# Performance work log

Measured on AMD Instinct MI355X. Metric: run time of the kernel, lower is better.

Reference implementation:

```python
import jax, jax.numpy as jnp
import numpy as np

N_NODES = 50000
N_EDGES = 800000
F_IN, F_MID, F_OUT = 256, 128, 40


def gcn_conv(x, W, b, src, dst, n_nodes):
    # GCNConv (PyG defaults): add self-loops, symmetric normalization,
    # linear transform, scatter-sum to targets, then bias.
    h = x @ W  # [N, F_out]
    loop = jnp.arange(n_nodes, dtype=src.dtype)
    s = jnp.concatenate([src, loop])  # sources incl. self-loops
    d = jnp.concatenate([dst, loop])  # targets incl. self-loops
    deg = jax.ops.segment_sum(jnp.ones_like(d, dtype=h.dtype), d, num_segments=n_nodes)
    dinv = jnp.where(deg > 0, jax.lax.rsqrt(deg), 0.0)
    norm = dinv[s] * dinv[d]  # [E+N]
    msgs = h[s] * norm[:, None]  # [E+N, F_out]
    out = jax.ops.segment_sum(msgs, d, num_segments=n_nodes)
    return out + b


def setup_inputs() -> dict:
    key = jax.random.key(0)
    ks = jax.random.split(key, 8)
    x = jax.random.normal(ks[0], (N_NODES, F_IN), dtype=jnp.float32)
    edge_index = jax.random.randint(ks[1], (2, N_EDGES), 0, N_NODES, dtype=jnp.int64)

    def glorot(k, fin, fout):
        lim = float(np.sqrt(6.0 / (fin + fout)))
        return jax.random.uniform(k, (fin, fout), jnp.float32, -lim, lim)

    return {
        "x": x,
        "edge_index": edge_index,
        "W_in": glorot(ks[2], F_IN, F_MID),
        "b_in": jnp.zeros((F_MID,), jnp.float32),
        "W_mid": glorot(ks[3], F_MID, F_MID),
        "b_mid": jnp.zeros((F_MID,), jnp.float32),
        "W_out": glorot(ks[4], F_MID, F_OUT),
        "b_out": jnp.zeros((F_OUT,), jnp.float32),
    }


def reference(x, edge_index, W_in, b_in, W_mid, b_mid, W_out, b_out):
    src, dst = edge_index[0], edge_index[1]
    n = x.shape[0]
    # conv_in -> relu (dropout is identity in eval mode)
    h = jax.nn.relu(gcn_conv(x, W_in, b_in, src, dst, n))
    # middle GCN layer -> relu
    h = jax.nn.relu(gcn_conv(h, W_mid, b_mid, src, dst, n))
    # conv_out -> log_softmax over classes
    h = gcn_conv(h, W_out, b_out, src, dst, n)
    return jax.nn.log_softmax(h, axis=-1)
```

## Files before the change

### kernel.cpp

```cpp
#include <hip/hip_runtime.h>
#include <hip/hip_bf16.h>
#include <math.h>


#define F_IN  256
#define F_MID 128
#define F_OUT 40
#define PSH   9
#define BCAP2 10240

typedef __attribute__((ext_vector_type(8))) short bf16x8;
typedef __attribute__((ext_vector_type(4))) float f32x4;

union FragU {
    bf16x8 v;
    __hip_bfloat162 h2[4];
    uint4 u;
    unsigned short s[8];
};

__device__ __forceinline__ unsigned int f2bf(float f) {
    unsigned int u = __float_as_uint(f);
    return (u + 0x7fffu + ((u >> 16) & 1u)) >> 16;
}
__device__ __forceinline__ float bf_lo(unsigned int u) { return __uint_as_float(u << 16); }
__device__ __forceinline__ float bf_hi(unsigned int u) { return __uint_as_float(u & 0xffff0000u); }

__global__ __launch_bounds__(256) void k_bucket_prep(const int* __restrict__ src,
                                                     const int* __restrict__ dst,
                                                     unsigned int* __restrict__ bkt,
                                                     int* __restrict__ bcur,
                                                     int E, int nbB,
                                                     const float* __restrict__ W1,
                                                     const float* __restrict__ W2,
                                                     const float* __restrict__ W3,
                                                     unsigned short* __restrict__ Wp1,
                                                     unsigned short* __restrict__ Wp2,
                                                     unsigned short* __restrict__ Wp3) {
    if (blockIdx.x >= (unsigned)nbB) {
        int t = (blockIdx.x - nbB) * 256 + threadIdx.x;
        const float* W; unsigned short* Wp; int M, Mp, kc, nn;
        if (t < 4096)      { W = W1; Wp = Wp1; M = 128; Mp = 128; kc = t >> 7; nn = t & 127; }
        else if (t < 6144) { t -= 4096; W = W2; Wp = Wp2; M = 128; Mp = 128; kc = t >> 7; nn = t & 127; }
        else if (t < 6912) { t -= 6144; W = W3; Wp = Wp3; M = 40;  Mp = 48;  kc = t / 48; nn = t % 48; }
        else return;
        FragU o;
#pragma unroll
        for (int j = 0; j < 8; ++j) {
            int k = kc * 8 + j;
            o.s[j] = (nn < M) ? (unsigned short)f2bf(W[k * M + nn]) : 0;
        }
        *(uint4*)&Wp[((size_t)kc * Mp + nn) * 8] = o.u;
        return;
    }
    __shared__ int hist[128], base[128], cur[128];
    const int ntiles = (E + 2047) >> 11;
    for (int tile = blockIdx.x; tile < ntiles; tile += nbB) {
        const int e0 = tile << 11;
        if (threadIdx.x < 128) { hist[threadIdx.x] = 0; cur[threadIdx.x] = 0; }
        __syncthreads();
        int myp[8];
        unsigned int mye[8];
#pragma unroll
        for (int j = 0; j < 8; ++j) {
            int e = e0 + j * 256 + threadIdx.x;
            myp[j] = -1;
            if (e < E) {
                int s = src[e], d = dst[e];
                int p = d >> PSH;
                myp[j] = p;
                mye[j] = ((unsigned int)d << 16) | (unsigned int)s;
                atomicAdd(&hist[p], 1);
            }
        }
        __syncthreads();
        if (threadIdx.x < 128)
            base[threadIdx.x] = atomicAdd(&bcur[threadIdx.x], hist[threadIdx.x]);
        __syncthreads();
#pragma unroll
        for (int j = 0; j < 8; ++j) {
            if (myp[j] >= 0) {
                int p = myp[j];
                int pos = base[p] + atomicAdd(&cur[p], 1);
                if (pos < BCAP2) bkt[(size_t)p * BCAP2 + pos] = mye[j];
            }
        }
        __syncthreads();
    }
}

__global__ __launch_bounds__(256) void k_gemm1_sort(const unsigned int* __restrict__ bkt,
                                                    const int* __restrict__ bcur,
                                                    int* __restrict__ rofs,
                                                    float* __restrict__ dinv,
                                                    unsigned short* __restrict__ csr,
                                                    int nbG, int npart,
                                                    const float* __restrict__ x,
                                                    const unsigned short* __restrict__ Wp1,
                                                    unsigned short* __restrict__ hn, int n) {
    if (blockIdx.x >= (unsigned)nbG) {
        __shared__ int hist[512];
        __shared__ int stmp[256];
        const int p = blockIdx.x - nbG;
        const int t = threadIdx.x;
        const int d0 = p << PSH;
        const int nd = min(512, n - d0);

        int bv = (t < p) ? bcur[t] : 0;
        bv = bv > BCAP2 ? BCAP2 : bv;
        stmp[t] = bv;
        hist[t] = 0; hist[t + 256] = 0;
        __syncthreads();
#pragma unroll
        for (int off = 128; off; off >>= 1) {
            if (t < off) stmp[t] += stmp[t + off];
            __syncthreads();
        }
        const int base = stmp[0];
        int np = bcur[p]; np = np > BCAP2 ? BCAP2 : np;
        const unsigned int* b = bkt + (size_t)p * BCAP2;

        for (int i = t; i < np; i += 256)
            atomicAdd(&hist[(int)(b[i] >> 16) - d0], 1);
        __syncthreads();

        const int h0 = hist[2 * t], h1 = hist[2 * t + 1];
        __syncthreads();
        stmp[t] = h0 + h1;
        __syncthreads();
#pragma unroll
        for (int off = 1; off < 256; off <<= 1) {
            int xx = (t >= off) ? stmp[t - off] : 0;
            __syncthreads();
            stmp[t] += xx;
            __syncthreads();
        }
        const int excl = stmp[t] - (h0 + h1);

        hist[2 * t] = excl;
        hist[2 * t + 1] = excl + h0;
        if (2 * t < nd) {
            rofs[d0 + 2 * t] = base + excl;
            dinv[d0 + 2 * t] = rsqrtf((float)(h0 + 1));
        }
        if (2 * t + 1 < nd) {
            rofs[d0 + 2 * t + 1] = base + excl + h0;
            dinv[d0 + 2 * t + 1] = rsqrtf((float)(h1 + 1));
        }
        if (p == npart - 1 && t == 0) rofs[n] = base + np;
        __syncthreads();

        for (int i = t; i < np; i += 256) {
            unsigned int en = b[i];
            int ld = (int)(en >> 16) - d0;
            int pos = atomicAdd(&hist[ld], 1);
            csr[base + pos] = (unsigned short)(en & 0xffffu);
        }
        return;
    }
    const int t = threadIdx.x;
    const int w = t >> 6, lane = t & 63, sub = lane & 15, q = lane >> 4;
    const int row0 = blockIdx.x * 64 + w * 16;
    const int row = row0 + sub;
    const bool rv = row < n;
    const float* ap = x + (size_t)row * 256;

    float4 xv[16];
    if (rv) {
#pragma unroll
        for (int j = 0; j < 16; ++j)
            xv[j] = *(const float4*)(ap + (j >> 1) * 32 + q * 8 + (j & 1) * 4);
    } else {
#pragma unroll
        for (int j = 0; j < 16; ++j) xv[j] = make_float4(0.f, 0.f, 0.f, 0.f);
    }

    f32x4 acc[8];
#pragma unroll
    for (int cg = 0; cg < 8; ++cg) acc[cg] = (f32x4)0.f;

#pragma unroll
    for (int kk = 0; kk < 8; ++kk) {
        FragU af;
        float4 f0 = xv[2 * kk];
        float4 f1 = xv[2 * kk + 1];
        af.h2[0] = __float22bfloat162_rn(make_float2(f0.x, f0.y));
        af.h2[1] = __float22bfloat162_rn(make_float2(f0.z, f0.w));
        af.h2[2] = __float22bfloat162_rn(make_float2(f1.x, f1.y));
        af.h2[3] = __float22bfloat162_rn(make_float2(f1.z, f1.w));
        const unsigned short* wrow = Wp1 + (size_t)((kk * 4 + q) * 128 + sub) * 8;
#pragma unroll
        for (int cg = 0; cg < 8; ++cg) {
            bf16x8 b = *(const bf16x8*)(wrow + cg * 16 * 8);
            acc[cg] = __builtin_amdgcn_mfma_f32_16x16x32_bf16(af.v, b, acc[cg], 0, 0, 0);
        }
    }

    const int rbase = row0 + q * 4;
#pragma unroll
    for (int cg = 0; cg < 8; ++cg)
#pragma unroll
        for (int r = 0; r < 4; ++r) {
            int rr = rbase + r;
            if (rr < n)
                hn[(size_t)rr * 128 + cg * 16 + sub] = (unsigned short)f2bf(acc[cg][r]);
        }
}

template <int K>
__global__ __launch_bounds__(256) void gemm_mfma_bf16A(const unsigned short* __restrict__ A,
                                                       const unsigned short* __restrict__ Wp,
                                                       unsigned short* __restrict__ hn, int n) {
    const int t = threadIdx.x;
    const int w = t >> 6, lane = t & 63, sub = lane & 15, q = lane >> 4;
    const int row0 = blockIdx.x * 64 + w * 16;
    const int row = row0 + sub;
    const bool rv = row < n;
    const unsigned short* ap = A + (size_t)row * K;

    uint4 xv[K / 32];
    if (rv) {
#pragma unroll
        for (int j = 0; j < K / 32; ++j)
            xv[j] = *(const uint4*)(ap + j * 32 + q * 8);
    } else {
#pragma unroll
        for (int j = 0; j < K / 32; ++j) xv[j] = make_uint4(0, 0, 0, 0);
    }

    f32x4 acc[8];
#pragma unroll
    for (int cg = 0; cg < 8; ++cg) acc[cg] = (f32x4)0.f;

#pragma unroll
    for (int kk = 0; kk < K / 32; ++kk) {
        FragU af; af.u = xv[kk];
        const unsigned short* wrow = Wp + (size_t)((kk * 4 + q) * 128 + sub) * 8;
#pragma unroll
        for (int cg = 0; cg < 8; ++cg) {
            bf16x8 b = *(const bf16x8*)(wrow + cg * 16 * 8);
            acc[cg] = __builtin_amdgcn_mfma_f32_16x16x32_bf16(af.v, b, acc[cg], 0, 0, 0);
        }
    }

    const int rbase = row0 + q * 4;
#pragma unroll
    for (int cg = 0; cg < 8; ++cg)
#pragma unroll
        for (int r = 0; r < 4; ++r) {
            int rr = rbase + r;
            if (rr < n)
                hn[(size_t)rr * 128 + cg * 16 + sub] = (unsigned short)f2bf(acc[cg][r]);
        }
}

__global__ __launch_bounds__(256) void gemm_mfma_m40(const unsigned short* __restrict__ A,
                                                     const unsigned short* __restrict__ Wp,
                                                     unsigned short* __restrict__ hn, int n) {
    const int K = 128;
    const int t = threadIdx.x;
    const int w = t >> 6, lane = t & 63, sub = lane & 15, q = lane >> 4;
    const int row0 = blockIdx.x * 64 + w * 16;
    const int row = row0 + sub;
    const bool rv = row < n;
    const unsigned short* ap = A + (size_t)row * K;

    uint4 xv[4];
    if (rv) {
#pragma unroll
        for (int j = 0; j < 4; ++j)
            xv[j] = *(const uint4*)(ap + j * 32 + q * 8);
    } else {
#pragma unroll
        for (int j = 0; j < 4; ++j) xv[j] = make_uint4(0, 0, 0, 0);
    }

    f32x4 acc[3];
#pragma unroll
    for (int cg = 0; cg < 3; ++cg) acc[cg] = (f32x4)0.f;

#pragma unroll
    for (int kk = 0; kk < 4; ++kk) {
        FragU af; af.u = xv[kk];
        const unsigned short* wrow = Wp + (size_t)((kk * 4 + q) * 48 + sub) * 8;
#pragma unroll
        for (int cg = 0; cg < 3; ++cg) {
            bf16x8 b = *(const bf16x8*)(wrow + cg * 16 * 8);
            acc[cg] = __builtin_amdgcn_mfma_f32_16x16x32_bf16(af.v, b, acc[cg], 0, 0, 0);
        }
    }

    const int rbase = row0 + q * 4;
#pragma unroll
    for (int cg = 0; cg < 3; ++cg) {
        int col = cg * 16 + sub;
        if (col < 40) {
#pragma unroll
            for (int r = 0; r < 4; ++r) {
                int rr = rbase + r;
                if (rr < n)
                    hn[(size_t)rr * 40 + col] = (unsigned short)f2bf(acc[cg][r]);
            }
        }
    }
}

__device__ __forceinline__ void acc_row(float* acc, uint4 u, float dv) {
    acc[0] += dv * bf_lo(u.x); acc[1] += dv * bf_hi(u.x);
    acc[2] += dv * bf_lo(u.y); acc[3] += dv * bf_hi(u.y);
    acc[4] += dv * bf_lo(u.z); acc[5] += dv * bf_hi(u.z);
    acc[6] += dv * bf_lo(u.w); acc[7] += dv * bf_hi(u.w);
}

__global__ __launch_bounds__(256) void agg128_bf16(const unsigned short* __restrict__ hn,
                                                   const int* __restrict__ rofs,
                                                   const unsigned short* __restrict__ csr,
                                                   const float* __restrict__ dinv,
                                                   const float* __restrict__ bias,
                                                   unsigned short* __restrict__ obf, int n) {
    int wid = (blockIdx.x * 256 + threadIdx.x) >> 6;
    if (wid >= n) return;
    const int v = wid;
    const int lane = threadIdx.x & 63;
    const int q = lane >> 4;
    const int sub = lane & 15;
    float acc[8];
#pragma unroll
    for (int k = 0; k < 8; ++k) acc[k] = 0.f;
    const int e0 = rofs[v];
    const int total = rofs[v + 1] - e0 + 1;
    int i = q;
    for (; i + 12 < total; i += 16) {
        int s0 = (i == 0) ? v : (int)csr[e0 + i - 1];
        int s1 = (int)csr[e0 + i + 3];
        int s2 = (int)csr[e0 + i + 7];
        int s3 = (int)csr[e0 + i + 11];
        float d0 = dinv[s0], d1 = dinv[s1], d2 = dinv[s2], d3 = dinv[s3];
        uint4 u0 = *(const uint4*)(hn + (size_t)s0 * 128 + sub * 8);
        uint4 u1 = *(const uint4*)(hn + (size_t)s1 * 128 + sub * 8);
        uint4 u2 = *(const uint4*)(hn + (size_t)s2 * 128 + sub * 8);
        uint4 u3 = *(const uint4*)(hn + (size_t)s3 * 128 + sub * 8);
        acc_row(acc, u0, d0); acc_row(acc, u1, d1);
        acc_row(acc, u2, d2); acc_row(acc, u3, d3);
    }
    for (; i < total; i += 4) {
        int s = (i == 0) ? v : (int)csr[e0 + i - 1];
        float d = dinv[s];
        uint4 u = *(const uint4*)(hn + (size_t)s * 128 + sub * 8);
        acc_row(acc, u, d);
    }
#pragma unroll
    for (int k = 0; k < 8; ++k) {
        acc[k] += __shfl_xor(acc[k], 16);
        acc[k] += __shfl_xor(acc[k], 32);
    }
    if (q == 0) {
        float dv = dinv[v];
        float4 b0 = *(const float4*)(bias + sub * 8);
        float4 b1 = *(const float4*)(bias + sub * 8 + 4);
        float o[8];
        o[0] = fmaxf(dv * acc[0] + b0.x, 0.f);
        o[1] = fmaxf(dv * acc[1] + b0.y, 0.f);
        o[2] = fmaxf(dv * acc[2] + b0.z, 0.f);
        o[3] = fmaxf(dv * acc[3] + b0.w, 0.f);
        o[4] = fmaxf(dv * acc[4] + b1.x, 0.f);
        o[5] = fmaxf(dv * acc[5] + b1.y, 0.f);
        o[6] = fmaxf(dv * acc[6] + b1.z, 0.f);
        o[7] = fmaxf(dv * acc[7] + b1.w, 0.f);
        uint4 pk;
        pk.x = f2bf(o[0]) | (f2bf(o[1]) << 16);
        pk.y = f2bf(o[2]) | (f2bf(o[3]) << 16);
        pk.z = f2bf(o[4]) | (f2bf(o[5]) << 16);
        pk.w = f2bf(o[6]) | (f2bf(o[7]) << 16);
        *(uint4*)(obf + (size_t)v * 128 + sub * 8) = pk;
    }
}

__global__ __launch_bounds__(256) void agg40_lsm_bf16(const unsigned short* __restrict__ hn,
                                                      const int* __restrict__ rofs,
                                                      const unsigned short* __restrict__ csr,
                                                      const float* __restrict__ dinv,
                                                      const float* __restrict__ bias,
                                                      float* __restrict__ out, int n) {
    int wid = (blockIdx.x * 256 + threadIdx.x) >> 6;
    if (wid >= n) return;
    const int v = wid;
    const int lane = threadIdx.x & 63;
    const int h = lane >> 5;
    const int sl = lane & 31;
    const bool act = sl < 20;
    float a0 = 0.f, a1 = 0.f;
    const int e0 = rofs[v];
    const int total = rofs[v + 1] - e0 + 1;
    int i = h;
    for (; i + 2 < total; i += 4) {
        int s0 = (i == 0) ? v : (int)csr[e0 + i - 1];
        int s1 = (int)csr[e0 + i + 1];
        if (act) {
            float d0 = dinv[s0], d1 = dinv[s1];
            unsigned int u0 = *(const unsigned int*)(hn + (size_t)s0 * 40 + sl * 2);
            unsigned int u1 = *(const unsigned int*)(hn + (size_t)s1 * 40 + sl * 2);
            a0 += d0 * bf_lo(u0) + d1 * bf_lo(u1);
            a1 += d0 * bf_hi(u0) + d1 * bf_hi(u1);
        }
    }
    if (i < total) {
        int s = (i == 0) ? v : (int)csr[e0 + i - 1];
        if (act) {
            float d = dinv[s];
            unsigned int u = *(const unsigned int*)(hn + (size_t)s * 40 + sl * 2);
            a0 += d * bf_lo(u);
            a1 += d * bf_hi(u);
        }
    }
    a0 += __shfl_xor(a0, 32);
    a1 += __shfl_xor(a1, 32);
    float dv = dinv[v];
    float v0 = act ? (dv * a0 + bias[sl * 2])     : -3.402823466e38f;
    float v1 = act ? (dv * a1 + bias[sl * 2 + 1]) : -3.402823466e38f;
    float m = fmaxf(v0, v1);
#pragma unroll
    for (int off = 16; off; off >>= 1) m = fmaxf(m, __shfl_xor(m, off));
    float p = act ? (__expf(v0 - m) + __expf(v1 - m)) : 0.f;
#pragma unroll
    for (int off = 16; off; off >>= 1) p += __shfl_xor(p, off);
    if (h == 0 && act) {
        float ls = __logf(p);
        *(float2*)(out + (size_t)v * 40 + sl * 2) = make_float2(v0 - m - ls, v1 - m - ls);
    }
}


extern "C" void kernel_launch(void* const* d_in, const int* in_sizes, int n_in,
                              void* d_out, int out_size, void* d_ws, size_t ws_size,
                              hipStream_t stream) {
    const float* x     = (const float*)d_in[0];
    const int*   ei    = (const int*)d_in[1];
    const float* W_in  = (const float*)d_in[2];
    const float* b_in  = (const float*)d_in[3];
    const float* W_mid = (const float*)d_in[4];
    const float* b_mid = (const float*)d_in[5];
    const float* W_out = (const float*)d_in[6];
    const float* b_out = (const float*)d_in[7];
    float* out = (float*)d_out;

    const int N = in_sizes[0] / F_IN;
    const int E = in_sizes[1] / 2;
    const int* srcp = ei;
    const int* dstp = ei + E;
    const int npart = (N + (1 << PSH) - 1) >> PSH;

    char* w = (char*)d_ws;
    unsigned short* hn  = (unsigned short*)w; w += (size_t)N * 128 * 2;
    unsigned short* obf = (unsigned short*)w; w += (size_t)N * 128 * 2;
    float* dinv = (float*)w; w += (size_t)N * 4;
    int* bcur   = (int*)w;   w += 512;
    int* rofs   = (int*)w;   w += (size_t)(N + 1) * 4 + 12;
    unsigned int* bkt = (unsigned int*)w; w += (size_t)npart * BCAP2 * 4;
    unsigned short* csr = (unsigned short*)w; w += (size_t)E * 2 + 2;
    unsigned short* Wp1 = (unsigned short*)((((size_t)w) + 15) & ~(size_t)15); w = (char*)Wp1 + 32 * 128 * 8 * 2;
    unsigned short* Wp2 = (unsigned short*)w; w += 16 * 128 * 8 * 2;
    unsigned short* Wp3 = (unsigned short*)w; w += 16 * 48 * 8 * 2;

    const int nbW = (N * 64 + 255) / 256;
    const int nbG = (N + 63) / 64;
    const int nbB = 384;

    hipMemsetAsync(bcur, 0, 512, stream);
    k_bucket_prep<<<nbB + 27, 256, 0, stream>>>(srcp, dstp, bkt, bcur, E, nbB,
                                                W_in, W_mid, W_out, Wp1, Wp2, Wp3);
    k_gemm1_sort<<<nbG + npart, 256, 0, stream>>>(bkt, bcur, rofs, dinv, csr,
                                                  nbG, npart, x, Wp1, hn, N);

    agg128_bf16<<<nbW, 256, 0, stream>>>(hn, rofs, csr, dinv, b_in, obf, N);
    gemm_mfma_bf16A<128><<<nbG, 256, 0, stream>>>(obf, Wp2, hn, N);
    agg128_bf16<<<nbW, 256, 0, stream>>>(hn, rofs, csr, dinv, b_mid, obf, N);
    gemm_mfma_m40<<<nbG, 256, 0, stream>>>(obf, Wp3, hn, N);
    agg40_lsm_bf16<<<nbW, 256, 0, stream>>>(hn, rofs, csr, dinv, b_out, out, N);
}
```

Measured before the change: 268.7 us.

## Reschedule preprocessing: fuse bucketing with GEMM1, split sort, vectorize MFMA stores

Replaces the memset and the bucket-prep kernel with a small init kernel, then runs the edge bucketing in the same launch as the first GEMM, followed by a separate sort kernel. The aim is to overlap bucketing with the layer-1 GEMM. Each bucketing block now handles 8192 edges in a single pass, and the sort loads entries in batches of 8. The MFMA operands are swapped so each lane holds 4 consecutive features of one row, which lets the output be written with packed 8-byte stores instead of scalar 2-byte stores. The risks are higher register pressure in the 32-entry bucket loop and the extra kernel launch.

```diff
diff --git a/kernel.cpp b/kernel.cpp
--- a/kernel.cpp
+++ b/kernel.cpp
@@ -26,141 +26,71 @@
 __device__ __forceinline__ float bf_lo(unsigned int u) { return __uint_as_float(u << 16); }
 __device__ __forceinline__ float bf_hi(unsigned int u) { return __uint_as_float(u & 0xffff0000u); }
 
-__global__ __launch_bounds__(256) void k_bucket_prep(const int* __restrict__ src,
-                                                     const int* __restrict__ dst,
-                                                     unsigned int* __restrict__ bkt,
-                                                     int* __restrict__ bcur,
-                                                     int E, int nbB,
-                                                     const float* __restrict__ W1,
-                                                     const float* __restrict__ W2,
-                                                     const float* __restrict__ W3,
-                                                     unsigned short* __restrict__ Wp1,
-                                                     unsigned short* __restrict__ Wp2,
-                                                     unsigned short* __restrict__ Wp3) {
-    if (blockIdx.x >= (unsigned)nbB) {
-        int t = (blockIdx.x - nbB) * 256 + threadIdx.x;
-        const float* W; unsigned short* Wp; int M, Mp, kc, nn;
-        if (t < 4096)      { W = W1; Wp = Wp1; M = 128; Mp = 128; kc = t >> 7; nn = t & 127; }
-        else if (t < 6144) { t -= 4096; W = W2; Wp = Wp2; M = 128; Mp = 128; kc = t >> 7; nn = t & 127; }
-        else if (t < 6912) { t -= 6144; W = W3; Wp = Wp3; M = 40;  Mp = 48;  kc = t / 48; nn = t % 48; }
-        else return;
-        FragU o;
-#pragma unroll
-        for (int j = 0; j < 8; ++j) {
-            int k = kc * 8 + j;
-            o.s[j] = (nn < M) ? (unsigned short)f2bf(W[k * M + nn]) : 0;
-        }
-        *(uint4*)&Wp[((size_t)kc * Mp + nn) * 8] = o.u;
+__global__ __launch_bounds__(256) void k_prep0(int* __restrict__ bcur,
+                                               const float* __restrict__ W1,
+                                               const float* __restrict__ W2,
+                                               const float* __restrict__ W3,
+                                               unsigned short* __restrict__ Wp1,
+                                               unsigned short* __restrict__ Wp2,
+                                               unsigned short* __restrict__ Wp3) {
+    if (blockIdx.x == 0) {
+        if (threadIdx.x < 128) bcur[threadIdx.x] = 0;
         return;
     }
-    __shared__ int hist[128], base[128], cur[128];
-    const int ntiles = (E + 2047) >> 11;
-    for (int tile = blockIdx.x; tile < ntiles; tile += nbB) {
-        const int e0 = tile << 11;
-        if (threadIdx.x < 128) { hist[threadIdx.x] = 0; cur[threadIdx.x] = 0; }
-        __syncthreads();
-        int myp[8];
-        unsigned int mye[8];
-#pragma unroll
-        for (int j = 0; j < 8; ++j) {
-            int e = e0 + j * 256 + threadIdx.x;
-            myp[j] = -1;
+    int t = (blockIdx.x - 1) * 256 + threadIdx.x;
+    const float* W; unsigned short* Wp; int M, Mp, kc, nn;
+    if (t < 4096)      { W = W1; Wp = Wp1; M = 128; Mp = 128; kc = t >> 7; nn = t & 127; }
+    else if (t < 6144) { t -= 4096; W = W2; Wp = Wp2; M = 128; Mp = 128; kc = t >> 7; nn = t & 127; }
+    else if (t < 6912) { t -= 6144; W = W3; Wp = Wp3; M = 40;  Mp = 48;  kc = t / 48; nn = t % 48; }
+    else return;
+    FragU o;
+#pragma unroll
+    for (int j = 0; j < 8; ++j) {
+        int k = kc * 8 + j;
+        o.s[j] = (nn < M) ? (unsigned short)f2bf(W[k * M + nn]) : 0;
+    }
+    *(uint4*)&Wp[((size_t)kc * Mp + nn) * 8] = o.u;
+}
+
+__global__ __launch_bounds__(256) void k_bucket_gemm1(const int* __restrict__ src,
+                                                      const int* __restrict__ dst,
+                                                      unsigned int* __restrict__ bkt,
+                                                      int* __restrict__ bcur,
+                                                      int E, int nbBkt,
+                                                      const float* __restrict__ x,
+                                                      const unsigned short* __restrict__ Wp1,
+                                                      unsigned short* __restrict__ hn, int n) {
+    if (blockIdx.x < (unsigned)nbBkt) {
+        __shared__ int hist[128], base[128], cur[128];
+        const int t = threadIdx.x;
+        if (t < 128) { hist[t] = 0; cur[t] = 0; }
+        __syncthreads();
+        const int e0 = blockIdx.x * 8192;
+        unsigned int mye[32];
+#pragma unroll
+        for (int j = 0; j < 32; ++j) {
+            int e = e0 + j * 256 + t;
             if (e < E) {
-                int s = src[e], d = dst[e];
-                int p = d >> PSH;
-                myp[j] = p;
-                mye[j] = ((unsigned int)d << 16) | (unsigned int)s;
-                atomicAdd(&hist[p], 1);
-            }
-        }
-        __syncthreads();
-        if (threadIdx.x < 128)
-            base[threadIdx.x] = atomicAdd(&bcur[threadIdx.x], hist[threadIdx.x]);
-        __syncthreads();
-#pragma unroll
-        for (int j = 0; j < 8; ++j) {
-            if (myp[j] >= 0) {
-                int p = myp[j];
+                mye[j] = ((unsigned int)dst[e] << 16) | (unsigned int)src[e];
+                atomicAdd(&hist[mye[j] >> (16 + PSH)], 1);
+            } else mye[j] = 0xffffffffu;
+        }
+        __syncthreads();
+        if (t < 128) base[t] = hist[t] ? atomicAdd(&bcur[t], hist[t]) : 0;
+        __syncthreads();
+#pragma unroll
+        for (int j = 0; j < 32; ++j) {
+            if (mye[j] != 0xffffffffu) {
+                int p = mye[j] >> (16 + PSH);
                 int pos = base[p] + atomicAdd(&cur[p], 1);
                 if (pos < BCAP2) bkt[(size_t)p * BCAP2 + pos] = mye[j];
             }
         }
-        __syncthreads();
-    }
-}
-
-__global__ __launch_bounds__(256) void k_gemm1_sort(const unsigned int* __restrict__ bkt,
-                                                    const int* __restrict__ bcur,
-                                                    int* __restrict__ rofs,
-                                                    float* __restrict__ dinv,
-                                                    unsigned short* __restrict__ csr,
-                                                    int nbG, int npart,
-                                                    const float* __restrict__ x,
-                                                    const unsigned short* __restrict__ Wp1,
-                                                    unsigned short* __restrict__ hn, int n) {
-    if (blockIdx.x >= (unsigned)nbG) {
-        __shared__ int hist[512];
-        __shared__ int stmp[256];
-        const int p = blockIdx.x - nbG;
-        const int t = threadIdx.x;
-        const int d0 = p << PSH;
-        const int nd = min(512, n - d0);
-
-        int bv = (t < p) ? bcur[t] : 0;
-        bv = bv > BCAP2 ? BCAP2 : bv;
-        stmp[t] = bv;
-        hist[t] = 0; hist[t + 256] = 0;
-        __syncthreads();
-#pragma unroll
-        for (int off = 128; off; off >>= 1) {
-            if (t < off) stmp[t] += stmp[t + off];
-            __syncthreads();
-        }
-        const int base = stmp[0];
-        int np = bcur[p]; np = np > BCAP2 ? BCAP2 : np;
-        const unsigned int* b = bkt + (size_t)p * BCAP2;
-
-        for (int i = t; i < np; i += 256)
-            atomicAdd(&hist[(int)(b[i] >> 16) - d0], 1);
-        __syncthreads();
-
-        const int h0 = hist[2 * t], h1 = hist[2 * t + 1];
-        __syncthreads();
-        stmp[t] = h0 + h1;
-        __syncthreads();
-#pragma unroll
-        for (int off = 1; off < 256; off <<= 1) {
-            int xx = (t >= off) ? stmp[t - off] : 0;
-            __syncthreads();
-            stmp[t] += xx;
-            __syncthreads();
-        }
-        const int excl = stmp[t] - (h0 + h1);
-
-        hist[2 * t] = excl;
-        hist[2 * t + 1] = excl + h0;
-        if (2 * t < nd) {
-            rofs[d0 + 2 * t] = base + excl;
-            dinv[d0 + 2 * t] = rsqrtf((float)(h0 + 1));
-        }
-        if (2 * t + 1 < nd) {
-            rofs[d0 + 2 * t + 1] = base + excl + h0;
-            dinv[d0 + 2 * t + 1] = rsqrtf((float)(h1 + 1));
-        }
-        if (p == npart - 1 && t == 0) rofs[n] = base + np;
-        __syncthreads();
-
-        for (int i = t; i < np; i += 256) {
-            unsigned int en = b[i];
-            int ld = (int)(en >> 16) - d0;
-            int pos = atomicAdd(&hist[ld], 1);
-            csr[base + pos] = (unsigned short)(en & 0xffffu);
-        }
         return;
     }
     const int t = threadIdx.x;
     const int w = t >> 6, lane = t & 63, sub = lane & 15, q = lane >> 4;
-    const int row0 = blockIdx.x * 64 + w * 16;
+    const int row0 = (blockIdx.x - nbBkt) * 64 + w * 16;
     const int row = row0 + sub;
     const bool rv = row < n;
     const float* ap = x + (size_t)row * 256;
@@ -192,19 +122,103 @@
 #pragma unroll
         for (int cg = 0; cg < 8; ++cg) {
             bf16x8 b = *(const bf16x8*)(wrow + cg * 16 * 8);
-            acc[cg] = __builtin_amdgcn_mfma_f32_16x16x32_bf16(af.v, b, acc[cg], 0, 0, 0);
-        }
-    }
-
-    const int rbase = row0 + q * 4;
-#pragma unroll
-    for (int cg = 0; cg < 8; ++cg)
-#pragma unroll
-        for (int r = 0; r < 4; ++r) {
-            int rr = rbase + r;
-            if (rr < n)
-                hn[(size_t)rr * 128 + cg * 16 + sub] = (unsigned short)f2bf(acc[cg][r]);
-        }
+            acc[cg] = __builtin_amdgcn_mfma_f32_16x16x32_bf16(b, af.v, acc[cg], 0, 0, 0);
+        }
+    }
+    if (rv) {
+#pragma unroll
+        for (int cg = 0; cg < 8; ++cg) {
+            uint2 pk;
+            pk.x = f2bf(acc[cg][0]) | (f2bf(acc[cg][1]) << 16);
+            pk.y = f2bf(acc[cg][2]) | (f2bf(acc[cg][3]) << 16);
+            *(uint2*)(hn + (size_t)row * 128 + cg * 16 + q * 4) = pk;
+        }
+    }
+}
+
+__global__ __launch_bounds__(256) void k_sort(const unsigned int* __restrict__ bkt,
+                                              const int* __restrict__ bcur,
+                                              int* __restrict__ rofs,
+                                              float* __restrict__ dinv,
+                                              unsigned short* __restrict__ csr,
+                                              int npart, int n) {
+    __shared__ int hist[512];
+    __shared__ int stmp[256];
+    const int p = blockIdx.x;
+    const int t = threadIdx.x;
+    const int d0 = p << PSH;
+    const int nd = min(512, n - d0);
+
+    int bv = (t < p) ? bcur[t] : 0;
+    bv = bv > BCAP2 ? BCAP2 : bv;
+    stmp[t] = bv;
+    hist[t] = 0; hist[t + 256] = 0;
+    __syncthreads();
+#pragma unroll
+    for (int off = 128; off; off >>= 1) {
+        if (t < off) stmp[t] += stmp[t + off];
+        __syncthreads();
+    }
+    const int base = stmp[0];
+    int np = bcur[p]; np = np > BCAP2 ? BCAP2 : np;
+    const unsigned int* b = bkt + (size_t)p * BCAP2;
+
+    for (int i0 = t; i0 < np; i0 += 2048) {
+        unsigned int ee[8];
+#pragma unroll
+        for (int j = 0; j < 8; ++j) {
+            int idx = i0 + j * 256;
+            ee[j] = (idx < np) ? b[idx] : 0xffffffffu;
+        }
+#pragma unroll
+        for (int j = 0; j < 8; ++j)
+            if (ee[j] != 0xffffffffu)
+                atomicAdd(&hist[(int)(ee[j] >> 16) - d0], 1);
+    }
+    __syncthreads();
+
+    const int h0 = hist[2 * t], h1 = hist[2 * t + 1];
+    __syncthreads();
+    stmp[t] = h0 + h1;
+    __syncthreads();
+#pragma unroll
+    for (int off = 1; off < 256; off <<= 1) {
+        int xx = (t >= off) ? stmp[t - off] : 0;
+        __syncthreads();
+        stmp[t] += xx;
+        __syncthreads();
+    }
+    const int excl = stmp[t] - (h0 + h1);
+
+    hist[2 * t] = excl;
+    hist[2 * t + 1] = excl + h0;
+    if (2 * t < nd) {
+        rofs[d0 + 2 * t] = base + excl;
+        dinv[d0 + 2 * t] = rsqrtf((float)(h0 + 1));
+    }
+    if (2 * t + 1 < nd) {
+        rofs[d0 + 2 * t + 1] = base + excl + h0;
+        dinv[d0 + 2 * t + 1] = rsqrtf((float)(h1 + 1));
+    }
+    if (p == npart - 1 && t == 0) rofs[n] = base + np;
+    __syncthreads();
+
+    for (int i0 = t; i0 < np; i0 += 2048) {
+        unsigned int ee[8];
+#pragma unroll
+        for (int j = 0; j < 8; ++j) {
+            int idx = i0 + j * 256;
+            ee[j] = (idx < np) ? b[idx] : 0xffffffffu;
+        }
+#pragma unroll
+        for (int j = 0; j < 8; ++j) {
+            if (ee[j] != 0xffffffffu) {
+                int ld = (int)(ee[j] >> 16) - d0;
+                int pos = atomicAdd(&hist[ld], 1);
+                csr[base + pos] = (unsigned short)(ee[j] & 0xffffu);
+            }
+        }
+    }
 }
 
 template <int K>
@@ -239,19 +253,19 @@
 #pragma unroll
         for (int cg = 0; cg < 8; ++cg) {
             bf16x8 b = *(const bf16x8*)(wrow + cg * 16 * 8);
-            acc[cg] = __builtin_amdgcn_mfma_f32_16x16x32_bf16(af.v, b, acc[cg], 0, 0, 0);
-        }
-    }
-
-    const int rbase = row0 + q * 4;
-#pragma unroll
-    for (int cg = 0; cg < 8; ++cg)
-#pragma unroll
-        for (int r = 0; r < 4; ++r) {
-            int rr = rbase + r;
-            if (rr < n)
-                hn[(size_t)rr * 128 + cg * 16 + sub] = (unsigned short)f2bf(acc[cg][r]);
-        }
+            acc[cg] = __builtin_amdgcn_mfma_f32_16x16x32_bf16(b, af.v, acc[cg], 0, 0, 0);
+        }
+    }
+
+    if (rv) {
+#pragma unroll
+        for (int cg = 0; cg < 8; ++cg) {
+            uint2 pk;
+            pk.x = f2bf(acc[cg][0]) | (f2bf(acc[cg][1]) << 16);
+            pk.y = f2bf(acc[cg][2]) | (f2bf(acc[cg][3]) << 16);
+            *(uint2*)(hn + (size_t)row * 128 + cg * 16 + q * 4) = pk;
+        }
+    }
 }
 
 __global__ __launch_bounds__(256) void gemm_mfma_m40(const unsigned short* __restrict__ A,
@@ -286,20 +300,19 @@
 #pragma unroll
         for (int cg = 0; cg < 3; ++cg) {
             bf16x8 b = *(const bf16x8*)(wrow + cg * 16 * 8);
-            acc[cg] = __builtin_amdgcn_mfma_f32_16x16x32_bf16(af.v, b, acc[cg], 0, 0, 0);
-        }
-    }
-
-    const int rbase = row0 + q * 4;
-#pragma unroll
-    for (int cg = 0; cg < 3; ++cg) {
-        int col = cg * 16 + sub;
-        if (col < 40) {
-#pragma unroll
-            for (int r = 0; r < 4; ++r) {
-                int rr = rbase + r;
-                if (rr < n)
-                    hn[(size_t)rr * 40 + col] = (unsigned short)f2bf(acc[cg][r]);
+            acc[cg] = __builtin_amdgcn_mfma_f32_16x16x32_bf16(b, af.v, acc[cg], 0, 0, 0);
+        }
+    }
+
+    if (rv) {
+#pragma unroll
+        for (int cg = 0; cg < 3; ++cg) {
+            int feat = cg * 16 + q * 4;
+            if (feat < 40) {
+                uint2 pk;
+                pk.x = f2bf(acc[cg][0]) | (f2bf(acc[cg][1]) << 16);
+                pk.y = f2bf(acc[cg][2]) | (f2bf(acc[cg][3]) << 16);
+                *(uint2*)(hn + (size_t)row * 40 + feat) = pk;
             }
         }
     }
@@ -464,13 +477,12 @@
 
     const int nbW = (N * 64 + 255) / 256;
     const int nbG = (N + 63) / 64;
-    const int nbB = 384;
-
-    hipMemsetAsync(bcur, 0, 512, stream);
-    k_bucket_prep<<<nbB + 27, 256, 0, stream>>>(srcp, dstp, bkt, bcur, E, nbB,
-                                                W_in, W_mid, W_out, Wp1, Wp2, Wp3);
-    k_gemm1_sort<<<nbG + npart, 256, 0, stream>>>(bkt, bcur, rofs, dinv, csr,
-                                                  nbG, npart, x, Wp1, hn, N);
+    const int nbBkt = (E + 8191) / 8192;
+
+    k_prep0<<<28, 256, 0, stream>>>(bcur, W_in, W_mid, W_out, Wp1, Wp2, Wp3);
+    k_bucket_gemm1<<<nbBkt + nbG, 256, 0, stream>>>(srcp, dstp, bkt, bcur, E, nbBkt,
+                                                    x, Wp1, hn, N);
+    k_sort<<<npart, 256, 0, stream>>>(bkt, bcur, rofs, dinv, csr, npart, N);
 
     agg128_bf16<<<nbW, 256, 0, stream>>>(hn, rofs, csr, dinv, b_in, obf, N);
     gemm_mfma_bf16A<128><<<nbG, 256, 0, stream>>>(obf, Wp2, hn, N);
```

Result: faster. 256.2 us (-4.6%).
